# Performance work log

Hardware: AMD Instinct MI355X
Metric: run time of the kernel (lower is better)

The kernel has to match this reference:

```python
import jax, jax.numpy as jnp
import numpy as np

B, T, D, H = 256, 512, 512, 512


def setup_inputs() -> dict:
    key = jax.random.key(0)
    k1, k2, k3, k4 = jax.random.split(key, 4)
    inputs = jax.random.normal(k1, (B, T, D), dtype=jnp.float32)
    lengths = jax.random.randint(k2, (B,), 0, T).astype(jnp.int32)
    # LSTM params. Flax nn.LSTMCell uses per-gate dense layers:
    #  input dense (with bias) and recurrent dense (no bias). Packing the
    #  four gates (i, f, g, o) into one matrix is mathematically identical.
    Wx = jax.random.normal(k3, (D, 4 * H), dtype=jnp.float32) * (1.0 / np.sqrt(D))
    Wh = jax.random.normal(k4, (H, 4 * H), dtype=jnp.float32) * (1.0 / np.sqrt(H))
    b = jnp.zeros((4 * H,), dtype=jnp.float32)
    return {"inputs": inputs, "lengths": lengths, "Wx": Wx, "Wh": Wh, "b": b}


def reference(inputs, lengths, Wx, Wh, b):
    batch = inputs.shape[0]
    hidden = Wh.shape[0]
    x_tbd = jnp.swapaxes(inputs, 0, 1)  # [T, B, D]

    def step(carry, x_t):
        c, h = carry
        # fused gate pre-activations: [B, 4H]
        z = x_t @ Wx + h @ Wh + b
        i, f, g, o = jnp.split(z, 4, axis=-1)
        i = jax.nn.sigmoid(i)
        f = jax.nn.sigmoid(f)
        g = jnp.tanh(g)
        o = jax.nn.sigmoid(o)
        c_new = f * c + i * g
        h_new = o * jnp.tanh(c_new)
        return (c_new, h_new), h_new

    c0 = jnp.zeros((batch, hidden), dtype=inputs.dtype)
    h0 = jnp.zeros((batch, hidden), dtype=inputs.dtype)
    _, hs = jax.lax.scan(step, (c0, h0), x_tbd)  # hs: [T, B, H]

    # select output at last valid timestep per example
    idx = jnp.maximum(0, lengths - 1)  # [B]
    return hs[idx, jnp.arange(batch), :]  # [B, H]
```

## Files before the change

### kernel.cpp

```cpp
#include <hip/hip_runtime.h>

#define Bb 256
#define Tt 512
#define Dd 512
#define Hh 512
#define KTOT 1024
#define FOURH 2048

typedef __attribute__((ext_vector_type(8))) short bf16x8;
typedef __attribute__((ext_vector_type(4))) float f32x4;

__device__ __forceinline__ unsigned short f2bf(float f) {
    union { float f; unsigned u; } x; x.f = f;
    unsigned u = x.u;
    unsigned r = u + 0x7FFFu + ((u >> 16) & 1u);
    return (unsigned short)(r >> 16);
}
__device__ __forceinline__ float bf2f(unsigned short s) {
    union { unsigned u; float f; } x; x.u = ((unsigned)s) << 16;
    return x.f;
}

__device__ __forceinline__ uint4 load16_sc01(const void* p) {
    uint4 v;
    asm volatile("global_load_dwordx4 %0, %1, off sc0 sc1" : "=v"(v) : "v"(p));
    return v;
}

__device__ __forceinline__ void i16_to_bf(int v, unsigned short& bh, unsigned short& bl) {
    int vh = v >> 8;
    int vl = v & 255;
    union { float f; unsigned u; } a, b;
    a.f = (float)vh * 0.0078125f;
    b.f = (float)vl * 3.0517578125e-05f;
    bh = (unsigned short)(a.u >> 16);
    bl = (unsigned short)(b.u >> 16);
}

__global__ void prep_w(const float* __restrict__ Wx, const float* __restrict__ Wh,
                       unsigned short* __restrict__ WT_hi, unsigned short* __restrict__ WT_lo) {
    __shared__ float tile[32][33];
    int n0 = (blockIdx.x & 63) * 32;
    int k0 = (blockIdx.x >> 6) * 32;
    int tx = threadIdx.x & 31;
    int ty = threadIdx.x >> 5;
    for (int q = 0; q < 4; ++q) {
        int k = k0 + ty + q * 8;
        int n = n0 + tx;
        float v = (k < Dd) ? Wx[(size_t)k * FOURH + n] : Wh[(size_t)(k - Dd) * FOURH + n];
        tile[ty + q * 8][tx] = v;
    }
    __syncthreads();
    for (int q = 0; q < 4; ++q) {
        int nl = ty + q * 8;
        int kl = tx;
        float v = tile[kl][nl];
        unsigned short hi = f2bf(v);
        unsigned short lo = f2bf(v - bf2f(hi));
        size_t o = (size_t)(n0 + nl) * KTOT + (size_t)(k0 + kl);
        WT_hi[o] = hi;
        WT_lo[o] = lo;
    }
}

__global__ void init_state3(char* __restrict__ ws, int persist) {
    long i = (long)blockIdx.x * blockDim.x + threadIdx.x;
    if (i < 98304) {
        *(uint4*)(ws + (8u << 20) + i * 16) = (uint4){0, 0, 0, 0};
    }
    if (persist && i < 4096) {
        ((unsigned int*)(ws + (8u << 20) + (1536u << 10)))[i] = 0u;
    }
}

__global__ __launch_bounds__(512) void lstm_persist12(
    const float* __restrict__ X, const int* __restrict__ lengths,
    const unsigned short* __restrict__ WT_hi, const unsigned short* __restrict__ WT_lo,
    const float* __restrict__ bias,
    short* __restrict__ h_i16,
    unsigned int* __restrict__ ctrl,
    float* __restrict__ out)
{
    __shared__ unsigned short HLDS[32768];
    __shared__ unsigned short XLDS[32768];
    __shared__ float zbuf[8][32][17];

    const int bx = blockIdx.x;
    const int group = bx & 7;
    const int slot = bx >> 3;
    const int rt = slot & 7;
    const int cs = slot >> 3;
    const int r0 = rt * 32;
    const int j0h = group * 64 + cs * 16;
    const int tid = threadIdx.x;
    const int w8 = tid >> 6;
    const int lane = tid & 63;
    const int l15 = lane & 15;
    const int q4 = lane >> 4;
    const int klo = q4 * 8;
    const int gate = w8 & 3;
    const int khalf = w8 >> 2;

    const size_t HB = (size_t)Bb * Hh;

    const int colg = gate * 512 + j0h + l15;
    const size_t bbase = (size_t)colg * KTOT + (size_t)khalf * 512;
    const unsigned short* bhp = &WT_hi[bbase];
    const unsigned short* blp = &WT_lo[bbase];

    const int xr = tid >> 4;
    const int xk0 = (tid & 15) * 32;
    const float* xbase = &X[((size_t)(r0 + xr) * Tt) * Dd + xk0];
    const int ksx = tid & 15;
    const int xmi = xr >> 4, xlr = xr & 15;

    const int er = tid >> 4;
    const int ej = tid & 15;
    const int row_g = r0 + er;
    const int col_h = j0h + ej;
    const size_t oidx = (size_t)row_g * Hh + col_h;
    int oT = lengths[row_g] - 1; if (oT < 0) oT = 0;
    const float b0 = bias[col_h], b1 = bias[512 + col_h],
                b2 = bias[1024 + col_h], b3 = bias[1536 + col_h];
    float creg = 0.f;

    const int wgIdx = group * 4 + cs;
    unsigned int* myflag = ctrl + ((size_t)(rt * 32 + wgIdx)) * 16;
    const unsigned int* flagbase = ctrl + (size_t)rt * 32 * 16;
    const unsigned int* pollp = flagbase + (size_t)(lane & 31) * 16;

    {
        const float* xp = xbase;
        float4 xv[8];
#pragma unroll
        for (int i = 0; i < 8; ++i) xv[i] = ((const float4*)xp)[i];
#pragma unroll
        for (int c2 = 0; c2 < 4; ++c2) {
            float vv[8];
            *(float4*)&vv[0] = xv[2 * c2];
            *(float4*)&vv[4] = xv[2 * c2 + 1];
            bf16x8 hv8, lv8;
#pragma unroll
            for (int e = 0; e < 8; ++e) {
                unsigned short hs = f2bf(vv[e]);
                hv8[e] = (short)hs;
                lv8[e] = (short)f2bf(vv[e] - bf2f(hs));
            }
            const int lnw = (c2 * 16 + xlr) ^ (ksx & 7);
            *(bf16x8*)&XLDS[(((0 * 2 + xmi) * 16 + ksx) * 64 + lnw) * 8] = hv8;
            *(bf16x8*)&XLDS[(((1 * 2 + xmi) * 16 + ksx) * 64 + lnw) * 8] = lv8;
        }
    }

    for (int t = 0; t < Tt; ++t) {
        const int p_r = t & 1;
        const short* hp_r = h_i16 + (size_t)p_r * HB;
        short* hp_w = h_i16 + (size_t)(p_r ^ 1) * HB;

        uint4 hb[4];
#pragma unroll
        for (int it = 0; it < 4; ++it) {
            const int c = it * 512 + tid;
            const int row = c >> 6, k8 = c & 63;
            hb[it] = load16_sc01(hp_r + (size_t)(r0 + row) * Hh + k8 * 8);
        }

        asm volatile("s_waitcnt vmcnt(0)" ::: "memory");
        __builtin_amdgcn_sched_barrier(0);

#pragma unroll
        for (int it = 0; it < 4; ++it) {
            const int c = it * 512 + tid;
            const int row = c >> 6, k8 = c & 63;
            const int ksh = k8 >> 2, qq = k8 & 3;
            const int mi = row >> 4, lr = row & 15;
            const uint4 q = hb[it];
            const unsigned qs[4] = {q.x, q.y, q.z, q.w};
            bf16x8 ahv, alv;
#pragma unroll
            for (int e = 0; e < 4; ++e) {
                const unsigned u = qs[e];
                unsigned short bh0, bl0, bh1, bl1;
                i16_to_bf((int)(short)(u & 0xffffu), bh0, bl0);
                i16_to_bf((int)(short)(u >> 16), bh1, bl1);
                ahv[2 * e] = (short)bh0; alv[2 * e] = (short)bl0;
                ahv[2 * e + 1] = (short)bh1; alv[2 * e + 1] = (short)bl1;
            }
            const int lnw = (qq * 16 + lr) ^ (ksh & 7);
            *(bf16x8*)&HLDS[(((0 * 2 + mi) * 16 + ksh) * 64 + lnw) * 8] = ahv;
            *(bf16x8*)&HLDS[(((1 * 2 + mi) * 16 + ksh) * 64 + lnw) * 8] = alv;
        }
        __syncthreads();

        const unsigned short* ALDS = khalf ? HLDS : XLDS;
        f32x4 acc[2][3];
#pragma unroll
        for (int mi = 0; mi < 2; ++mi)
#pragma unroll
            for (int s = 0; s < 3; ++s)
                acc[mi][s] = (f32x4){0.f, 0.f, 0.f, 0.f};

#pragma unroll
        for (int ks = 0; ks < 16; ++ks) {
            const int kk = ks * 32 + klo;
            const bf16x8 bh = *(const bf16x8*)&bhp[kk];
            const bf16x8 bl = *(const bf16x8*)&blp[kk];
            const int lnr = lane ^ (ks & 7);
#pragma unroll
            for (int mi = 0; mi < 2; ++mi) {
                const bf16x8 ah = *(const bf16x8*)&ALDS[(((0 * 2 + mi) * 16 + ks) * 64 + lnr) * 8];
                const bf16x8 al = *(const bf16x8*)&ALDS[(((1 * 2 + mi) * 16 + ks) * 64 + lnr) * 8];
                acc[mi][0] = __builtin_amdgcn_mfma_f32_16x16x32_bf16(ah, bh, acc[mi][0], 0, 0, 0);
                acc[mi][1] = __builtin_amdgcn_mfma_f32_16x16x32_bf16(ah, bl, acc[mi][1], 0, 0, 0);
                acc[mi][2] = __builtin_amdgcn_mfma_f32_16x16x32_bf16(al, bh, acc[mi][2], 0, 0, 0);
            }
        }

#pragma unroll
        for (int mi = 0; mi < 2; ++mi) {
            const f32x4 z = acc[mi][0] + acc[mi][1] + acc[mi][2];
#pragma unroll
            for (int r = 0; r < 4; ++r)
                zbuf[w8][mi * 16 + q4 * 4 + r][l15] = z[r];
        }
        __syncthreads();

        float zi = zbuf[0][er][ej] + zbuf[4][er][ej] + b0;
        float zf = zbuf[1][er][ej] + zbuf[5][er][ej] + b1;
        float zg = zbuf[2][er][ej] + zbuf[6][er][ej] + b2;
        float zo = zbuf[3][er][ej] + zbuf[7][er][ej] + b3;
        float ig = 1.f / (1.f + expf(-zi));
        float fg = 1.f / (1.f + expf(-zf));
        float gg = tanhf(zg);
        float og = 1.f / (1.f + expf(-zo));
        float cn = fg * creg + ig * gg;
        creg = cn;
        float hn = og * tanhf(cn);
        int vi = __float2int_rn(hn * 32768.f);
        vi = vi > 32767 ? 32767 : (vi < -32767 ? -32767 : vi);
        __hip_atomic_store(&hp_w[oidx], (short)vi, __ATOMIC_RELAXED, __HIP_MEMORY_SCOPE_SYSTEM);
        if (t == oT) out[oidx] = hn;

        if (t < Tt - 1) {
            asm volatile("s_waitcnt vmcnt(0)" ::: "memory");
            __syncthreads();
            if (tid == 0)
                __hip_atomic_store(myflag, (unsigned)(t + 1), __ATOMIC_RELAXED,
                                   __HIP_MEMORY_SCOPE_SYSTEM);

            {
                const float* xp = xbase + (size_t)(t + 1) * Dd;
                float4 xv[8];
#pragma unroll
                for (int i = 0; i < 8; ++i) xv[i] = ((const float4*)xp)[i];
#pragma unroll
                for (int c2 = 0; c2 < 4; ++c2) {
                    float vv[8];
                    *(float4*)&vv[0] = xv[2 * c2];
                    *(float4*)&vv[4] = xv[2 * c2 + 1];
                    bf16x8 hv8, lv8;
#pragma unroll
                    for (int e = 0; e < 8; ++e) {
                        unsigned short hs = f2bf(vv[e]);
                        hv8[e] = (short)hs;
                        lv8[e] = (short)f2bf(vv[e] - bf2f(hs));
                    }
                    const int lnw = (c2 * 16 + xlr) ^ (ksx & 7);
                    *(bf16x8*)&XLDS[(((0 * 2 + xmi) * 16 + ksx) * 64 + lnw) * 8] = hv8;
                    *(bf16x8*)&XLDS[(((1 * 2 + xmi) * 16 + ksx) * 64 + lnw) * 8] = lv8;
                }
            }

            if (w8 == 0) {
                while (true) {
                    unsigned v = __hip_atomic_load(pollp, __ATOMIC_RELAXED,
                                                   __HIP_MEMORY_SCOPE_SYSTEM);
                    if (__all(v >= (unsigned)(t + 1))) break;
                    __builtin_amdgcn_s_sleep(2);
                }
            }
            __syncthreads();
        }
    }
}

__global__ __launch_bounds__(512) void lstm_step4(
    const float* __restrict__ X, const int* __restrict__ lengths,
    const unsigned short* __restrict__ WT_hi, const unsigned short* __restrict__ WT_lo,
    const float* __restrict__ bias,
    float* __restrict__ c_st,
    const unsigned short* __restrict__ h_r_hi, const unsigned short* __restrict__ h_r_lo,
    unsigned short* __restrict__ h_w_hi, unsigned short* __restrict__ h_w_lo,
    float* __restrict__ out, int t)
{
    __shared__ float zbuf[8][16][17];

    const int bx = blockIdx.x;
    const int xcd = bx & 7;
    const int rem = bx >> 3;
    const int m0 = (rem & 15) * 16;
    const int col_group = xcd * 4 + (rem >> 4);
    const int hc0 = col_group * 16;
    const int tid = threadIdx.x;
    const int w8 = tid >> 6;
    const int lane = tid & 63;
    const int gate = w8 & 3;
    const int khalf = w8 >> 2;

    f32x4 ahh = (f32x4){0,0,0,0}, ahl = (f32x4){0,0,0,0}, alh = (f32x4){0,0,0,0};

    const int colk = gate * 512 + hc0 + (lane & 15);
    const size_t bbase = (size_t)colk * KTOT;
    const int klo = (lane >> 4) * 8;
    const int row = m0 + (lane & 15);

    if (khalf == 0) {
        const float* xrow = &X[((size_t)row * Tt + t) * Dd];
        const unsigned short* bhp = &WT_hi[bbase];
        const unsigned short* blp = &WT_lo[bbase];
#pragma unroll
        for (int ks = 0; ks < 16; ++ks) {
            const int kk = ks * 32 + klo;
            const float4 v0 = *(const float4*)&xrow[kk];
            const float4 v1 = *(const float4*)&xrow[kk + 4];
            float vv[8] = {v0.x, v0.y, v0.z, v0.w, v1.x, v1.y, v1.z, v1.w};
            bf16x8 ah, al;
#pragma unroll
            for (int e = 0; e < 8; ++e) {
                unsigned short hi = f2bf(vv[e]);
                ah[e] = (short)hi;
                al[e] = (short)f2bf(vv[e] - bf2f(hi));
            }
            const bf16x8 bh = *(const bf16x8*)&bhp[kk];
            const bf16x8 bl = *(const bf16x8*)&blp[kk];
            ahh = __builtin_amdgcn_mfma_f32_16x16x32_bf16(ah, bh, ahh, 0, 0, 0);
            ahl = __builtin_amdgcn_mfma_f32_16x16x32_bf16(ah, bl, ahl, 0, 0, 0);
            alh = __builtin_amdgcn_mfma_f32_16x16x32_bf16(al, bh, alh, 0, 0, 0);
        }
    } else {
        const unsigned short* hrh = &h_r_hi[(size_t)row * Hh];
        const unsigned short* hrl = &h_r_lo[(size_t)row * Hh];
        const unsigned short* bhp = &WT_hi[bbase + 512];
        const unsigned short* blp = &WT_lo[bbase + 512];
#pragma unroll
        for (int ks = 0; ks < 16; ++ks) {
            const int kk = ks * 32 + klo;
            const bf16x8 ah = *(const bf16x8*)&hrh[kk];
            const bf16x8 al = *(const bf16x8*)&hrl[kk];
            const bf16x8 bh = *(const bf16x8*)&bhp[kk];
            const bf16x8 bl = *(const bf16x8*)&blp[kk];
            ahh = __builtin_amdgcn_mfma_f32_16x16x32_bf16(ah, bh, ahh, 0, 0, 0);
            ahl = __builtin_amdgcn_mfma_f32_16x16x32_bf16(ah, bl, ahl, 0, 0, 0);
            alh = __builtin_amdgcn_mfma_f32_16x16x32_bf16(al, bh, alh, 0, 0, 0);
        }
    }

    const f32x4 z = ahh + ahl + alh;
#pragma unroll
    for (int r = 0; r < 4; ++r)
        zbuf[w8][(lane >> 4) * 4 + r][lane & 15] = z[r];
    __syncthreads();

    if (tid < 256) {
        const int r = tid >> 4;
        const int j = tid & 15;
        const int row_g = m0 + r;
        const int col_g = hc0 + j;
        float zi = zbuf[0][r][j] + zbuf[4][r][j] + bias[col_g];
        float zf = zbuf[1][r][j] + zbuf[5][r][j] + bias[512 + col_g];
        float zg = zbuf[2][r][j] + zbuf[6][r][j] + bias[1024 + col_g];
        float zo = zbuf[3][r][j] + zbuf[7][r][j] + bias[1536 + col_g];
        float ig = 1.f / (1.f + expf(-zi));
        float fg = 1.f / (1.f + expf(-zf));
        float gg = tanhf(zg);
        float og = 1.f / (1.f + expf(-zo));
        const size_t idx = (size_t)row_g * Hh + col_g;
        float cn = fg * c_st[idx] + ig * gg;
        float hn = og * tanhf(cn);
        c_st[idx] = cn;
        unsigned short hh = f2bf(hn);
        h_w_hi[idx] = hh;
        h_w_lo[idx] = f2bf(hn - bf2f(hh));
        int len = lengths[row_g];
        int oidx = len - 1; if (oidx < 0) oidx = 0;
        if (t == oidx) out[idx] = hn;
    }
}

extern "C" void kernel_launch(void* const* d_in, const int* in_sizes, int n_in,
                              void* d_out, int out_size, void* d_ws, size_t ws_size,
                              hipStream_t stream) {
    const float* X = (const float*)d_in[0];
    const int* lengths = (const int*)d_in[1];
    const float* Wx = (const float*)d_in[2];
    const float* Wh = (const float*)d_in[3];
    const float* bias = (const float*)d_in[4];
    float* out = (float*)d_out;

    char* ws = (char*)d_ws;
    unsigned short* WT_hi = (unsigned short*)ws;
    unsigned short* WT_lo = (unsigned short*)(ws + (4u << 20));
    short* h_i16 = (short*)(ws + (8u << 20));
    unsigned int* ctrl = (unsigned int*)(ws + (8u << 20) + (1536u << 10));
    float* c_st = (float*)(ws + (8u << 20));
    unsigned short* h_base = (unsigned short*)(ws + (8u << 20) + (512u << 10));
    const size_t HB = (size_t)Bb * Hh;
    unsigned short* h_hi0 = h_base;
    unsigned short* h_lo0 = h_base + HB;
    unsigned short* h_hi1 = h_base + 2 * HB;
    unsigned short* h_lo1 = h_base + 3 * HB;

    const size_t NEED_PERSIST = (8u << 20) + (1536u << 10) + 32768u;
    const int can_persist = (ws_size >= NEED_PERSIST) ? 1 : 0;

    hipLaunchKernelGGL(prep_w, dim3(2048), dim3(256), 0, stream, Wx, Wh, WT_hi, WT_lo);
    hipLaunchKernelGGL(init_state3, dim3(512), dim3(256), 0, stream, ws, can_persist);

    hipError_t err = hipErrorUnknown;
    if (can_persist) {
        void* args[] = { (void*)&X, (void*)&lengths, (void*)&WT_hi, (void*)&WT_lo,
                         (void*)&bias, (void*)&h_i16, (void*)&ctrl, (void*)&out };
        err = hipLaunchCooperativeKernel((const void*)lstm_persist12,
                                         dim3(256), dim3(512), args, 0, stream);
    }
    if (err != hipSuccess) {
        for (int t = 0; t < Tt; ++t) {
            const bool even = (t & 1) == 0;
            hipLaunchKernelGGL(lstm_step4, dim3(512), dim3(512), 0, stream,
                               X, lengths, WT_hi, WT_lo, bias, c_st,
                               even ? h_hi0 : h_hi1, even ? h_lo0 : h_lo1,
                               even ? h_hi1 : h_hi0, even ? h_lo1 : h_lo0,
                               out, t);
        }
    }
}
```

Measured before the change: 6.112 ms.

## Replace flag barrier with tagged hidden-state values for per-element readiness polling

Removes the per-workgroup flag counters and the group-wide poll barrier. Each hidden value now carries a 1-bit parity tag in its LSB, and readers spin on the h data itself, reloading only stale chunks until all tags match the expected phase. The next step's h loads are issued right after the store, before the X conversion, so their latency overlaps. The cost is one bit of hidden-state quantization precision (15-bit instead of 16-bit) and a reliance on tag parity, which depends on double buffering to avoid ABA confusion.

```diff
diff --git a/kernel.cpp b/kernel.cpp
--- a/kernel.cpp
+++ b/kernel.cpp
@@ -27,12 +27,13 @@
     return v;
 }
 
-__device__ __forceinline__ void i16_to_bf(int v, unsigned short& bh, unsigned short& bl) {
-    int vh = v >> 8;
-    int vl = v & 255;
+__device__ __forceinline__ void s16tag_to_bf(int s, unsigned short& bh, unsigned short& bl) {
+    int vq = s >> 1;
+    int vh = vq >> 7;
+    int vl = vq & 127;
     union { float f; unsigned u; } a, b;
     a.f = (float)vh * 0.0078125f;
-    b.f = (float)vl * 3.0517578125e-05f;
+    b.f = (float)vl * 6.103515625e-05f;
     bh = (unsigned short)(a.u >> 16);
     bl = (unsigned short)(b.u >> 16);
 }
@@ -63,22 +64,21 @@
     }
 }
 
-__global__ void init_state3(char* __restrict__ ws, int persist) {
+__global__ void init_state5(char* __restrict__ ws, int persist) {
     long i = (long)blockIdx.x * blockDim.x + threadIdx.x;
     if (i < 98304) {
-        *(uint4*)(ws + (8u << 20) + i * 16) = (uint4){0, 0, 0, 0};
-    }
-    if (persist && i < 4096) {
-        ((unsigned int*)(ws + (8u << 20) + (1536u << 10)))[i] = 0u;
-    }
-}
-
-__global__ __launch_bounds__(512) void lstm_persist12(
+        uint4 v = (uint4){0, 0, 0, 0};
+        if (persist && i >= 16384 && i < 32768)
+            v = (uint4){0x00010001u, 0x00010001u, 0x00010001u, 0x00010001u};
+        *(uint4*)(ws + (8u << 20) + i * 16) = v;
+    }
+}
+
+__global__ __launch_bounds__(512) void lstm_persist14(
     const float* __restrict__ X, const int* __restrict__ lengths,
     const unsigned short* __restrict__ WT_hi, const unsigned short* __restrict__ WT_lo,
     const float* __restrict__ bias,
     short* __restrict__ h_i16,
-    unsigned int* __restrict__ ctrl,
     float* __restrict__ out)
 {
     __shared__ unsigned short HLDS[32768];
@@ -124,11 +124,6 @@
                 b2 = bias[1024 + col_h], b3 = bias[1536 + col_h];
     float creg = 0.f;
 
-    const int wgIdx = group * 4 + cs;
-    unsigned int* myflag = ctrl + ((size_t)(rt * 32 + wgIdx)) * 16;
-    const unsigned int* flagbase = ctrl + (size_t)rt * 32 * 16;
-    const unsigned int* pollp = flagbase + (size_t)(lane & 31) * 16;
-
     {
         const float* xp = xbase;
         float4 xv[8];
@@ -152,21 +147,45 @@
         }
     }
 
+    uint4 hb[4];
+    {
+        const short* hp0 = h_i16;
+#pragma unroll
+        for (int it = 0; it < 4; ++it) {
+            const int c = it * 512 + tid;
+            const int row = c >> 6, k8 = c & 63;
+            hb[it] = load16_sc01(hp0 + (size_t)(r0 + row) * Hh + k8 * 8);
+        }
+    }
+
     for (int t = 0; t < Tt; ++t) {
         const int p_r = t & 1;
         const short* hp_r = h_i16 + (size_t)p_r * HB;
         short* hp_w = h_i16 + (size_t)(p_r ^ 1) * HB;
-
-        uint4 hb[4];
-#pragma unroll
-        for (int it = 0; it < 4; ++it) {
-            const int c = it * 512 + tid;
-            const int row = c >> 6, k8 = c & 63;
-            hb[it] = load16_sc01(hp_r + (size_t)(r0 + row) * Hh + k8 * 8);
-        }
-
-        asm volatile("s_waitcnt vmcnt(0)" ::: "memory");
-        __builtin_amdgcn_sched_barrier(0);
+        const unsigned expTag = (unsigned)((t >> 1) & 1);
+        const unsigned tagpat = expTag ? 0x00010001u : 0u;
+
+        while (true) {
+            asm volatile("s_waitcnt vmcnt(0)" ::: "memory");
+            __builtin_amdgcn_sched_barrier(0);
+            unsigned stale = 0;
+#pragma unroll
+            for (int it = 0; it < 4; ++it) {
+                unsigned d = ((hb[it].x ^ tagpat) | (hb[it].y ^ tagpat) |
+                              (hb[it].z ^ tagpat) | (hb[it].w ^ tagpat)) & 0x00010001u;
+                if (d) stale |= (1u << it);
+            }
+            if (!__any(stale != 0)) break;
+#pragma unroll
+            for (int it = 0; it < 4; ++it) {
+                if (stale & (1u << it)) {
+                    const int c = it * 512 + tid;
+                    const int row = c >> 6, k8 = c & 63;
+                    hb[it] = load16_sc01(hp_r + (size_t)(r0 + row) * Hh + k8 * 8);
+                }
+            }
+            __builtin_amdgcn_s_sleep(4);
+        }
 
 #pragma unroll
         for (int it = 0; it < 4; ++it) {
@@ -181,8 +200,8 @@
             for (int e = 0; e < 4; ++e) {
                 const unsigned u = qs[e];
                 unsigned short bh0, bl0, bh1, bl1;
-                i16_to_bf((int)(short)(u & 0xffffu), bh0, bl0);
-                i16_to_bf((int)(short)(u >> 16), bh1, bl1);
+                s16tag_to_bf((int)(short)(u & 0xffffu), bh0, bl0);
+                s16tag_to_bf((int)(short)(u >> 16), bh1, bl1);
                 ahv[2 * e] = (short)bh0; alv[2 * e] = (short)bl0;
                 ahv[2 * e + 1] = (short)bh1; alv[2 * e + 1] = (short)bl1;
             }
@@ -236,50 +255,42 @@
         float cn = fg * creg + ig * gg;
         creg = cn;
         float hn = og * tanhf(cn);
-        int vi = __float2int_rn(hn * 32768.f);
-        vi = vi > 32767 ? 32767 : (vi < -32767 ? -32767 : vi);
-        __hip_atomic_store(&hp_w[oidx], (short)vi, __ATOMIC_RELAXED, __HIP_MEMORY_SCOPE_SYSTEM);
+        int vi = __float2int_rn(hn * 16384.f);
+        vi = vi > 16383 ? 16383 : (vi < -16383 ? -16383 : vi);
+        const unsigned tagNext = (unsigned)(((t + 1) >> 1) & 1);
+        short sv = (short)((vi << 1) | (int)tagNext);
+        __hip_atomic_store(&hp_w[oidx], sv, __ATOMIC_RELAXED, __HIP_MEMORY_SCOPE_SYSTEM);
         if (t == oT) out[oidx] = hn;
 
         if (t < Tt - 1) {
-            asm volatile("s_waitcnt vmcnt(0)" ::: "memory");
-            __syncthreads();
-            if (tid == 0)
-                __hip_atomic_store(myflag, (unsigned)(t + 1), __ATOMIC_RELAXED,
-                                   __HIP_MEMORY_SCOPE_SYSTEM);
-
-            {
-                const float* xp = xbase + (size_t)(t + 1) * Dd;
-                float4 xv[8];
-#pragma unroll
-                for (int i = 0; i < 8; ++i) xv[i] = ((const float4*)xp)[i];
-#pragma unroll
-                for (int c2 = 0; c2 < 4; ++c2) {
-                    float vv[8];
-                    *(float4*)&vv[0] = xv[2 * c2];
-                    *(float4*)&vv[4] = xv[2 * c2 + 1];
-                    bf16x8 hv8, lv8;
-#pragma unroll
-                    for (int e = 0; e < 8; ++e) {
-                        unsigned short hs = f2bf(vv[e]);
-                        hv8[e] = (short)hs;
-                        lv8[e] = (short)f2bf(vv[e] - bf2f(hs));
-                    }
-                    const int lnw = (c2 * 16 + xlr) ^ (ksx & 7);
-                    *(bf16x8*)&XLDS[(((0 * 2 + xmi) * 16 + ksx) * 64 + lnw) * 8] = hv8;
-                    *(bf16x8*)&XLDS[(((1 * 2 + xmi) * 16 + ksx) * 64 + lnw) * 8] = lv8;
+            const short* hp_n = h_i16 + (size_t)((t + 1) & 1) * HB;
+#pragma unroll
+            for (int it = 0; it < 4; ++it) {
+                const int c = it * 512 + tid;
+                const int row = c >> 6, k8 = c & 63;
+                hb[it] = load16_sc01(hp_n + (size_t)(r0 + row) * Hh + k8 * 8);
+            }
+
+            const float* xp = xbase + (size_t)(t + 1) * Dd;
+            float4 xv[8];
+#pragma unroll
+            for (int i = 0; i < 8; ++i) xv[i] = ((const float4*)xp)[i];
+#pragma unroll
+            for (int c2 = 0; c2 < 4; ++c2) {
+                float vv[8];
+                *(float4*)&vv[0] = xv[2 * c2];
+                *(float4*)&vv[4] = xv[2 * c2 + 1];
+                bf16x8 hv8, lv8;
+#pragma unroll
+                for (int e = 0; e < 8; ++e) {
+                    unsigned short hs = f2bf(vv[e]);
+                    hv8[e] = (short)hs;
+                    lv8[e] = (short)f2bf(vv[e] - bf2f(hs));
                 }
-            }
-
-            if (w8 == 0) {
-                while (true) {
-                    unsigned v = __hip_atomic_load(pollp, __ATOMIC_RELAXED,
-                                                   __HIP_MEMORY_SCOPE_SYSTEM);
-                    if (__all(v >= (unsigned)(t + 1))) break;
-                    __builtin_amdgcn_s_sleep(2);
-                }
-            }
-            __syncthreads();
+                const int lnw = (c2 * 16 + xlr) ^ (ksx & 7);
+                *(bf16x8*)&XLDS[(((0 * 2 + xmi) * 16 + ksx) * 64 + lnw) * 8] = hv8;
+                *(bf16x8*)&XLDS[(((1 * 2 + xmi) * 16 + ksx) * 64 + lnw) * 8] = lv8;
+            }
         }
     }
 }
@@ -401,7 +412,6 @@
     unsigned short* WT_hi = (unsigned short*)ws;
     unsigned short* WT_lo = (unsigned short*)(ws + (4u << 20));
     short* h_i16 = (short*)(ws + (8u << 20));
-    unsigned int* ctrl = (unsigned int*)(ws + (8u << 20) + (1536u << 10));
     float* c_st = (float*)(ws + (8u << 20));
     unsigned short* h_base = (unsigned short*)(ws + (8u << 20) + (512u << 10));
     const size_t HB = (size_t)Bb * Hh;
@@ -414,13 +424,13 @@
     const int can_persist = (ws_size >= NEED_PERSIST) ? 1 : 0;
 
     hipLaunchKernelGGL(prep_w, dim3(2048), dim3(256), 0, stream, Wx, Wh, WT_hi, WT_lo);
-    hipLaunchKernelGGL(init_state3, dim3(512), dim3(256), 0, stream, ws, can_persist);
+    hipLaunchKernelGGL(init_state5, dim3(512), dim3(256), 0, stream, ws, can_persist);
 
     hipError_t err = hipErrorUnknown;
     if (can_persist) {
         void* args[] = { (void*)&X, (void*)&lengths, (void*)&WT_hi, (void*)&WT_lo,
-                         (void*)&bias, (void*)&h_i16, (void*)&ctrl, (void*)&out };
-        err = hipLaunchCooperativeKernel((const void*)lstm_persist12,
+                         (void*)&bias, (void*)&h_i16, (void*)&out };
+        err = hipLaunchCooperativeKernel((const void*)lstm_persist14,
                                          dim3(256), dim3(512), args, 0, stream);
     }
     if (err != hipSuccess) {
```

New measurement: 6.417 ms. +5.0%, slower.

## Split recurrent h load into two halves to overlap conversion with MFMA

Applied to the files above, without the earlier changes.

Each step's h-state load is split into two K-halves. The first half is waited on, converted and staged into LDS. The h-path warps then compute on it while the second half's loads are still in flight, and the x-path warps run their full 16-step product. This is meant to hide the global-memory latency of the second half of h behind MFMA work. It adds an extra __syncthreads per timestep and uneven work between the x and h warp groups.

```diff
diff --git a/kernel.cpp b/kernel.cpp
--- a/kernel.cpp
+++ b/kernel.cpp
@@ -73,7 +73,7 @@
     }
 }
 
-__global__ __launch_bounds__(512) void lstm_persist12(
+__global__ __launch_bounds__(512) void lstm_persist15(
     const float* __restrict__ X, const int* __restrict__ lengths,
     const unsigned short* __restrict__ WT_hi, const unsigned short* __restrict__ WT_lo,
     const float* __restrict__ bias,
@@ -114,6 +114,11 @@
     const int ksx = tid & 15;
     const int xmi = xr >> 4, xlr = xr & 15;
 
+    const int hrow0 = (2 * tid) >> 5;
+    const int hrow1 = (2 * tid + 1) >> 5;
+    const int hk0 = (2 * tid) & 31;
+    const int hk1 = (2 * tid + 1) & 31;
+
     const int er = tid >> 4;
     const int ej = tid & 15;
     const int row_g = r0 + er;
@@ -158,23 +163,20 @@
         short* hp_w = h_i16 + (size_t)(p_r ^ 1) * HB;
 
         uint4 hb[4];
-#pragma unroll
-        for (int it = 0; it < 4; ++it) {
-            const int c = it * 512 + tid;
-            const int row = c >> 6, k8 = c & 63;
-            hb[it] = load16_sc01(hp_r + (size_t)(r0 + row) * Hh + k8 * 8);
-        }
-
-        asm volatile("s_waitcnt vmcnt(0)" ::: "memory");
+        hb[0] = load16_sc01(hp_r + (size_t)(r0 + hrow0) * Hh + hk0 * 8);
+        hb[1] = load16_sc01(hp_r + (size_t)(r0 + hrow1) * Hh + hk1 * 8);
+        hb[2] = load16_sc01(hp_r + (size_t)(r0 + hrow0) * Hh + (32 + hk0) * 8);
+        hb[3] = load16_sc01(hp_r + (size_t)(r0 + hrow1) * Hh + (32 + hk1) * 8);
+
+        asm volatile("s_waitcnt vmcnt(2)" ::: "memory");
         __builtin_amdgcn_sched_barrier(0);
-
-#pragma unroll
-        for (int it = 0; it < 4; ++it) {
-            const int c = it * 512 + tid;
-            const int row = c >> 6, k8 = c & 63;
+#pragma unroll
+        for (int b = 0; b < 2; ++b) {
+            const int row = b ? hrow1 : hrow0;
+            const int k8 = b ? hk1 : hk0;
             const int ksh = k8 >> 2, qq = k8 & 3;
             const int mi = row >> 4, lr = row & 15;
-            const uint4 q = hb[it];
+            const uint4 q = hb[b];
             const unsigned qs[4] = {q.x, q.y, q.z, q.w};
             bf16x8 ahv, alv;
 #pragma unroll
@@ -192,7 +194,6 @@
         }
         __syncthreads();
 
-        const unsigned short* ALDS = khalf ? HLDS : XLDS;
         f32x4 acc[2][3];
 #pragma unroll
         for (int mi = 0; mi < 2; ++mi)
@@ -200,28 +201,96 @@
             for (int s = 0; s < 3; ++s)
                 acc[mi][s] = (f32x4){0.f, 0.f, 0.f, 0.f};
 
-#pragma unroll
-        for (int ks = 0; ks < 16; ++ks) {
-            const int kk = ks * 32 + klo;
-            const bf16x8 bh = *(const bf16x8*)&bhp[kk];
-            const bf16x8 bl = *(const bf16x8*)&blp[kk];
-            const int lnr = lane ^ (ks & 7);
+        if (khalf == 0) {
+#pragma unroll
+            for (int ks = 0; ks < 16; ++ks) {
+                const int kk = ks * 32 + klo;
+                const bf16x8 bh = *(const bf16x8*)&bhp[kk];
+                const bf16x8 bl = *(const bf16x8*)&blp[kk];
+                const int lnr = lane ^ (ks & 7);
+#pragma unroll
+                for (int mi = 0; mi < 2; ++mi) {
+                    const bf16x8 ah = *(const bf16x8*)&XLDS[(((0 * 2 + mi) * 16 + ks) * 64 + lnr) * 8];
+                    const bf16x8 al = *(const bf16x8*)&XLDS[(((1 * 2 + mi) * 16 + ks) * 64 + lnr) * 8];
+                    acc[mi][0] = __builtin_amdgcn_mfma_f32_16x16x32_bf16(ah, bh, acc[mi][0], 0, 0, 0);
+                    acc[mi][1] = __builtin_amdgcn_mfma_f32_16x16x32_bf16(ah, bl, acc[mi][1], 0, 0, 0);
+                    acc[mi][2] = __builtin_amdgcn_mfma_f32_16x16x32_bf16(al, bh, acc[mi][2], 0, 0, 0);
+                }
+            }
 #pragma unroll
             for (int mi = 0; mi < 2; ++mi) {
-                const bf16x8 ah = *(const bf16x8*)&ALDS[(((0 * 2 + mi) * 16 + ks) * 64 + lnr) * 8];
-                const bf16x8 al = *(const bf16x8*)&ALDS[(((1 * 2 + mi) * 16 + ks) * 64 + lnr) * 8];
-                acc[mi][0] = __builtin_amdgcn_mfma_f32_16x16x32_bf16(ah, bh, acc[mi][0], 0, 0, 0);
-                acc[mi][1] = __builtin_amdgcn_mfma_f32_16x16x32_bf16(ah, bl, acc[mi][1], 0, 0, 0);
-                acc[mi][2] = __builtin_amdgcn_mfma_f32_16x16x32_bf16(al, bh, acc[mi][2], 0, 0, 0);
-            }
-        }
-
-#pragma unroll
-        for (int mi = 0; mi < 2; ++mi) {
-            const f32x4 z = acc[mi][0] + acc[mi][1] + acc[mi][2];
-#pragma unroll
-            for (int r = 0; r < 4; ++r)
-                zbuf[w8][mi * 16 + q4 * 4 + r][l15] = z[r];
+                const f32x4 z = acc[mi][0] + acc[mi][1] + acc[mi][2];
+#pragma unroll
+                for (int r = 0; r < 4; ++r)
+                    zbuf[w8][mi * 16 + q4 * 4 + r][l15] = z[r];
+            }
+        } else {
+#pragma unroll
+            for (int ks = 0; ks < 8; ++ks) {
+                const int kk = ks * 32 + klo;
+                const bf16x8 bh = *(const bf16x8*)&bhp[kk];
+                const bf16x8 bl = *(const bf16x8*)&blp[kk];
+                const int lnr = lane ^ (ks & 7);
+#pragma unroll
+                for (int mi = 0; mi < 2; ++mi) {
+                    const bf16x8 ah = *(const bf16x8*)&HLDS[(((0 * 2 + mi) * 16 + ks) * 64 + lnr) * 8];
+                    const bf16x8 al = *(const bf16x8*)&HLDS[(((1 * 2 + mi) * 16 + ks) * 64 + lnr) * 8];
+                    acc[mi][0] = __builtin_amdgcn_mfma_f32_16x16x32_bf16(ah, bh, acc[mi][0], 0, 0, 0);
+                    acc[mi][1] = __builtin_amdgcn_mfma_f32_16x16x32_bf16(ah, bl, acc[mi][1], 0, 0, 0);
+                    acc[mi][2] = __builtin_amdgcn_mfma_f32_16x16x32_bf16(al, bh, acc[mi][2], 0, 0, 0);
+                }
+            }
+        }
+
+        asm volatile("s_waitcnt vmcnt(0)" ::: "memory");
+        __builtin_amdgcn_sched_barrier(0);
+#pragma unroll
+        for (int b = 0; b < 2; ++b) {
+            const int row = b ? hrow1 : hrow0;
+            const int k8 = 32 + (b ? hk1 : hk0);
+            const int ksh = k8 >> 2, qq = k8 & 3;
+            const int mi = row >> 4, lr = row & 15;
+            const uint4 q = hb[2 + b];
+            const unsigned qs[4] = {q.x, q.y, q.z, q.w};
+            bf16x8 ahv, alv;
+#pragma unroll
+            for (int e = 0; e < 4; ++e) {
+                const unsigned u = qs[e];
+                unsigned short bh0, bl0, bh1, bl1;
+                i16_to_bf((int)(short)(u & 0xffffu), bh0, bl0);
+                i16_to_bf((int)(short)(u >> 16), bh1, bl1);
+                ahv[2 * e] = (short)bh0; alv[2 * e] = (short)bl0;
+                ahv[2 * e + 1] = (short)bh1; alv[2 * e + 1] = (short)bl1;
+            }
+            const int lnw = (qq * 16 + lr) ^ (ksh & 7);
+            *(bf16x8*)&HLDS[(((0 * 2 + mi) * 16 + ksh) * 64 + lnw) * 8] = ahv;
+            *(bf16x8*)&HLDS[(((1 * 2 + mi) * 16 + ksh) * 64 + lnw) * 8] = alv;
+        }
+        __syncthreads();
+
+        if (khalf == 1) {
+#pragma unroll
+            for (int ks = 8; ks < 16; ++ks) {
+                const int kk = ks * 32 + klo;
+                const bf16x8 bh = *(const bf16x8*)&bhp[kk];
+                const bf16x8 bl = *(const bf16x8*)&blp[kk];
+                const int lnr = lane ^ (ks & 7);
+#pragma unroll
+                for (int mi = 0; mi < 2; ++mi) {
+                    const bf16x8 ah = *(const bf16x8*)&HLDS[(((0 * 2 + mi) * 16 + ks) * 64 + lnr) * 8];
+                    const bf16x8 al = *(const bf16x8*)&HLDS[(((1 * 2 + mi) * 16 + ks) * 64 + lnr) * 8];
+                    acc[mi][0] = __builtin_amdgcn_mfma_f32_16x16x32_bf16(ah, bh, acc[mi][0], 0, 0, 0);
+                    acc[mi][1] = __builtin_amdgcn_mfma_f32_16x16x32_bf16(ah, bl, acc[mi][1], 0, 0, 0);
+                    acc[mi][2] = __builtin_amdgcn_mfma_f32_16x16x32_bf16(al, bh, acc[mi][2], 0, 0, 0);
+                }
+            }
+#pragma unroll
+            for (int mi = 0; mi < 2; ++mi) {
+                const f32x4 z = acc[mi][0] + acc[mi][1] + acc[mi][2];
+#pragma unroll
+                for (int r = 0; r < 4; ++r)
+                    zbuf[w8][mi * 16 + q4 * 4 + r][l15] = z[r];
+            }
         }
         __syncthreads();
 
@@ -420,7 +489,7 @@
     if (can_persist) {
         void* args[] = { (void*)&X, (void*)&lengths, (void*)&WT_hi, (void*)&WT_lo,
                          (void*)&bias, (void*)&h_i16, (void*)&ctrl, (void*)&out };
-        err = hipLaunchCooperativeKernel((const void*)lstm_persist12,
+        err = hipLaunchCooperativeKernel((const void*)lstm_persist15,
                                          dim3(256), dim3(512), args, 0, stream);
     }
     if (err != hipSuccess) {
```

After: 6.099 ms. About the same (-0.2%).

## Move input-projection GEMM off the recurrent critical path into the barrier wait

Applied to the files above, without the earlier changes.

The per-step work is restructured so the x·Wx partial products for step t+1 are computed by waves 1-7 while wave 0 spins on the grid barrier, and stored in a separate zxbuf. After the barrier only the h·Wh GEMM remains on the critical path, split across all 8 waves over K. The next h tile load is also issued right after the barrier, overlapping with wave 0's late x GEMM. This adds extra LDS syncs, a second z buffer, and a serial x GEMM on wave 0 after the barrier, which could delay the next step.

```diff
diff --git a/kernel.cpp b/kernel.cpp
--- a/kernel.cpp
+++ b/kernel.cpp
@@ -73,7 +73,7 @@
     }
 }
 
-__global__ __launch_bounds__(512) void lstm_persist12(
+__global__ __launch_bounds__(512) void lstm_persist16(
     const float* __restrict__ X, const int* __restrict__ lengths,
     const unsigned short* __restrict__ WT_hi, const unsigned short* __restrict__ WT_lo,
     const float* __restrict__ bias,
@@ -81,9 +81,9 @@
     unsigned int* __restrict__ ctrl,
     float* __restrict__ out)
 {
-    __shared__ unsigned short HLDS[32768];
-    __shared__ unsigned short XLDS[32768];
+    __shared__ unsigned short ALDS[32768];
     __shared__ float zbuf[8][32][17];
+    __shared__ float zxbuf[8][32][17];
 
     const int bx = blockIdx.x;
     const int group = bx & 7;
@@ -99,14 +99,15 @@
     const int q4 = lane >> 4;
     const int klo = q4 * 8;
     const int gate = w8 & 3;
-    const int khalf = w8 >> 2;
+    const int ksub = w8 >> 2;
 
     const size_t HB = (size_t)Bb * Hh;
 
     const int colg = gate * 512 + j0h + l15;
-    const size_t bbase = (size_t)colg * KTOT + (size_t)khalf * 512;
-    const unsigned short* bhp = &WT_hi[bbase];
-    const unsigned short* blp = &WT_lo[bbase];
+    const unsigned short* bhp_h = &WT_hi[(size_t)colg * KTOT + 512];
+    const unsigned short* blp_h = &WT_lo[(size_t)colg * KTOT + 512];
+    const unsigned short* bhp_x = &WT_hi[(size_t)colg * KTOT];
+    const unsigned short* blp_x = &WT_lo[(size_t)colg * KTOT];
 
     const int xr = tid >> 4;
     const int xk0 = (tid & 15) * 32;
@@ -147,24 +148,53 @@
                 lv8[e] = (short)f2bf(vv[e] - bf2f(hs));
             }
             const int lnw = (c2 * 16 + xlr) ^ (ksx & 7);
-            *(bf16x8*)&XLDS[(((0 * 2 + xmi) * 16 + ksx) * 64 + lnw) * 8] = hv8;
-            *(bf16x8*)&XLDS[(((1 * 2 + xmi) * 16 + ksx) * 64 + lnw) * 8] = lv8;
-        }
+            *(bf16x8*)&ALDS[(((0 * 2 + xmi) * 16 + ksx) * 64 + lnw) * 8] = hv8;
+            *(bf16x8*)&ALDS[(((1 * 2 + xmi) * 16 + ksx) * 64 + lnw) * 8] = lv8;
+        }
+    }
+    __syncthreads();
+    {
+        f32x4 acc[2][3];
+#pragma unroll
+        for (int mi = 0; mi < 2; ++mi)
+#pragma unroll
+            for (int s = 0; s < 3; ++s) acc[mi][s] = (f32x4){0, 0, 0, 0};
+#pragma unroll
+        for (int j = 0; j < 8; ++j) {
+            const int ks = ksub * 8 + j;
+            const int kk = ks * 32 + klo;
+            const bf16x8 bh = *(const bf16x8*)&bhp_x[kk];
+            const bf16x8 bl = *(const bf16x8*)&blp_x[kk];
+            const int lnr = lane ^ (ks & 7);
+#pragma unroll
+            for (int mi = 0; mi < 2; ++mi) {
+                const bf16x8 ah = *(const bf16x8*)&ALDS[(((0 * 2 + mi) * 16 + ks) * 64 + lnr) * 8];
+                const bf16x8 al = *(const bf16x8*)&ALDS[(((1 * 2 + mi) * 16 + ks) * 64 + lnr) * 8];
+                acc[mi][0] = __builtin_amdgcn_mfma_f32_16x16x32_bf16(ah, bh, acc[mi][0], 0, 0, 0);
+                acc[mi][1] = __builtin_amdgcn_mfma_f32_16x16x32_bf16(ah, bl, acc[mi][1], 0, 0, 0);
+                acc[mi][2] = __builtin_amdgcn_mfma_f32_16x16x32_bf16(al, bh, acc[mi][2], 0, 0, 0);
+            }
+        }
+#pragma unroll
+        for (int mi = 0; mi < 2; ++mi) {
+            const f32x4 z = acc[mi][0] + acc[mi][1] + acc[mi][2];
+#pragma unroll
+            for (int r = 0; r < 4; ++r)
+                zxbuf[w8][mi * 16 + q4 * 4 + r][l15] = z[r];
+        }
+    }
+    uint4 hb[4];
+#pragma unroll
+    for (int it = 0; it < 4; ++it) {
+        const int c = it * 512 + tid;
+        const int row = c >> 6, k8 = c & 63;
+        hb[it] = load16_sc01(h_i16 + (size_t)(r0 + row) * Hh + k8 * 8);
     }
 
     for (int t = 0; t < Tt; ++t) {
-        const int p_r = t & 1;
-        const short* hp_r = h_i16 + (size_t)p_r * HB;
-        short* hp_w = h_i16 + (size_t)(p_r ^ 1) * HB;
-
-        uint4 hb[4];
-#pragma unroll
-        for (int it = 0; it < 4; ++it) {
-            const int c = it * 512 + tid;
-            const int row = c >> 6, k8 = c & 63;
-            hb[it] = load16_sc01(hp_r + (size_t)(r0 + row) * Hh + k8 * 8);
-        }
-
+        short* hp_w = h_i16 + (size_t)((t ^ 1) & 1) * HB;
+
+        __syncthreads();
         asm volatile("s_waitcnt vmcnt(0)" ::: "memory");
         __builtin_amdgcn_sched_barrier(0);
 
@@ -187,48 +217,47 @@
                 ahv[2 * e + 1] = (short)bh1; alv[2 * e + 1] = (short)bl1;
             }
             const int lnw = (qq * 16 + lr) ^ (ksh & 7);
-            *(bf16x8*)&HLDS[(((0 * 2 + mi) * 16 + ksh) * 64 + lnw) * 8] = ahv;
-            *(bf16x8*)&HLDS[(((1 * 2 + mi) * 16 + ksh) * 64 + lnw) * 8] = alv;
+            *(bf16x8*)&ALDS[(((0 * 2 + mi) * 16 + ksh) * 64 + lnw) * 8] = ahv;
+            *(bf16x8*)&ALDS[(((1 * 2 + mi) * 16 + ksh) * 64 + lnw) * 8] = alv;
         }
         __syncthreads();
 
-        const unsigned short* ALDS = khalf ? HLDS : XLDS;
-        f32x4 acc[2][3];
-#pragma unroll
-        for (int mi = 0; mi < 2; ++mi)
-#pragma unroll
-            for (int s = 0; s < 3; ++s)
-                acc[mi][s] = (f32x4){0.f, 0.f, 0.f, 0.f};
-
-#pragma unroll
-        for (int ks = 0; ks < 16; ++ks) {
-            const int kk = ks * 32 + klo;
-            const bf16x8 bh = *(const bf16x8*)&bhp[kk];
-            const bf16x8 bl = *(const bf16x8*)&blp[kk];
-            const int lnr = lane ^ (ks & 7);
+        {
+            f32x4 acc[2][3];
+#pragma unroll
+            for (int mi = 0; mi < 2; ++mi)
+#pragma unroll
+                for (int s = 0; s < 3; ++s) acc[mi][s] = (f32x4){0, 0, 0, 0};
+#pragma unroll
+            for (int j = 0; j < 8; ++j) {
+                const int ks = ksub * 8 + j;
+                const int kk = ks * 32 + klo;
+                const bf16x8 bh = *(const bf16x8*)&bhp_h[kk];
+                const bf16x8 bl = *(const bf16x8*)&blp_h[kk];
+                const int lnr = lane ^ (ks & 7);
+#pragma unroll
+                for (int mi = 0; mi < 2; ++mi) {
+                    const bf16x8 ah = *(const bf16x8*)&ALDS[(((0 * 2 + mi) * 16 + ks) * 64 + lnr) * 8];
+                    const bf16x8 al = *(const bf16x8*)&ALDS[(((1 * 2 + mi) * 16 + ks) * 64 + lnr) * 8];
+                    acc[mi][0] = __builtin_amdgcn_mfma_f32_16x16x32_bf16(ah, bh, acc[mi][0], 0, 0, 0);
+                    acc[mi][1] = __builtin_amdgcn_mfma_f32_16x16x32_bf16(ah, bl, acc[mi][1], 0, 0, 0);
+                    acc[mi][2] = __builtin_amdgcn_mfma_f32_16x16x32_bf16(al, bh, acc[mi][2], 0, 0, 0);
+                }
+            }
 #pragma unroll
             for (int mi = 0; mi < 2; ++mi) {
-                const bf16x8 ah = *(const bf16x8*)&ALDS[(((0 * 2 + mi) * 16 + ks) * 64 + lnr) * 8];
-                const bf16x8 al = *(const bf16x8*)&ALDS[(((1 * 2 + mi) * 16 + ks) * 64 + lnr) * 8];
-                acc[mi][0] = __builtin_amdgcn_mfma_f32_16x16x32_bf16(ah, bh, acc[mi][0], 0, 0, 0);
-                acc[mi][1] = __builtin_amdgcn_mfma_f32_16x16x32_bf16(ah, bl, acc[mi][1], 0, 0, 0);
-                acc[mi][2] = __builtin_amdgcn_mfma_f32_16x16x32_bf16(al, bh, acc[mi][2], 0, 0, 0);
-            }
-        }
-
-#pragma unroll
-        for (int mi = 0; mi < 2; ++mi) {
-            const f32x4 z = acc[mi][0] + acc[mi][1] + acc[mi][2];
-#pragma unroll
-            for (int r = 0; r < 4; ++r)
-                zbuf[w8][mi * 16 + q4 * 4 + r][l15] = z[r];
+                const f32x4 z = acc[mi][0] + acc[mi][1] + acc[mi][2];
+#pragma unroll
+                for (int r = 0; r < 4; ++r)
+                    zbuf[w8][mi * 16 + q4 * 4 + r][l15] = z[r];
+            }
         }
         __syncthreads();
 
-        float zi = zbuf[0][er][ej] + zbuf[4][er][ej] + b0;
-        float zf = zbuf[1][er][ej] + zbuf[5][er][ej] + b1;
-        float zg = zbuf[2][er][ej] + zbuf[6][er][ej] + b2;
-        float zo = zbuf[3][er][ej] + zbuf[7][er][ej] + b3;
+        float zi = zbuf[0][er][ej] + zbuf[4][er][ej] + zxbuf[0][er][ej] + zxbuf[4][er][ej] + b0;
+        float zf = zbuf[1][er][ej] + zbuf[5][er][ej] + zxbuf[1][er][ej] + zxbuf[5][er][ej] + b1;
+        float zg = zbuf[2][er][ej] + zbuf[6][er][ej] + zxbuf[2][er][ej] + zxbuf[6][er][ej] + b2;
+        float zo = zbuf[3][er][ej] + zbuf[7][er][ej] + zxbuf[3][er][ej] + zxbuf[7][er][ej] + b3;
         float ig = 1.f / (1.f + expf(-zi));
         float fg = 1.f / (1.f + expf(-zf));
         float gg = tanhf(zg);
@@ -266,10 +295,17 @@
                         lv8[e] = (short)f2bf(vv[e] - bf2f(hs));
                     }
                     const int lnw = (c2 * 16 + xlr) ^ (ksx & 7);
-                    *(bf16x8*)&XLDS[(((0 * 2 + xmi) * 16 + ksx) * 64 + lnw) * 8] = hv8;
-                    *(bf16x8*)&XLDS[(((1 * 2 + xmi) * 16 + ksx) * 64 + lnw) * 8] = lv8;
-                }
-            }
+                    *(bf16x8*)&ALDS[(((0 * 2 + xmi) * 16 + ksx) * 64 + lnw) * 8] = hv8;
+                    *(bf16x8*)&ALDS[(((1 * 2 + xmi) * 16 + ksx) * 64 + lnw) * 8] = lv8;
+                }
+            }
+            __syncthreads();
+
+            f32x4 acc[2][3];
+#pragma unroll
+            for (int mi = 0; mi < 2; ++mi)
+#pragma unroll
+                for (int s = 0; s < 3; ++s) acc[mi][s] = (f32x4){0, 0, 0, 0};
 
             if (w8 == 0) {
                 while (true) {
@@ -278,8 +314,66 @@
                     if (__all(v >= (unsigned)(t + 1))) break;
                     __builtin_amdgcn_s_sleep(2);
                 }
+            } else {
+#pragma unroll
+                for (int j = 0; j < 8; ++j) {
+                    const int ks = ksub * 8 + j;
+                    const int kk = ks * 32 + klo;
+                    const bf16x8 bh = *(const bf16x8*)&bhp_x[kk];
+                    const bf16x8 bl = *(const bf16x8*)&blp_x[kk];
+                    const int lnr = lane ^ (ks & 7);
+#pragma unroll
+                    for (int mi = 0; mi < 2; ++mi) {
+                        const bf16x8 ah = *(const bf16x8*)&ALDS[(((0 * 2 + mi) * 16 + ks) * 64 + lnr) * 8];
+                        const bf16x8 al = *(const bf16x8*)&ALDS[(((1 * 2 + mi) * 16 + ks) * 64 + lnr) * 8];
+                        acc[mi][0] = __builtin_amdgcn_mfma_f32_16x16x32_bf16(ah, bh, acc[mi][0], 0, 0, 0);
+                        acc[mi][1] = __builtin_amdgcn_mfma_f32_16x16x32_bf16(ah, bl, acc[mi][1], 0, 0, 0);
+                        acc[mi][2] = __builtin_amdgcn_mfma_f32_16x16x32_bf16(al, bh, acc[mi][2], 0, 0, 0);
+                    }
+                }
+#pragma unroll
+                for (int mi = 0; mi < 2; ++mi) {
+                    const f32x4 z = acc[mi][0] + acc[mi][1] + acc[mi][2];
+#pragma unroll
+                    for (int r = 0; r < 4; ++r)
+                        zxbuf[w8][mi * 16 + q4 * 4 + r][l15] = z[r];
+                }
             }
             __syncthreads();
+
+            const short* hp_n = h_i16 + (size_t)((t + 1) & 1) * HB;
+#pragma unroll
+            for (int it = 0; it < 4; ++it) {
+                const int c = it * 512 + tid;
+                const int row = c >> 6, k8 = c & 63;
+                hb[it] = load16_sc01(hp_n + (size_t)(r0 + row) * Hh + k8 * 8);
+            }
+
+            if (w8 == 0) {
+#pragma unroll
+                for (int j = 0; j < 8; ++j) {
+                    const int ks = ksub * 8 + j;
+                    const int kk = ks * 32 + klo;
+                    const bf16x8 bh = *(const bf16x8*)&bhp_x[kk];
+                    const bf16x8 bl = *(const bf16x8*)&blp_x[kk];
+                    const int lnr = lane ^ (ks & 7);
+#pragma unroll
+                    for (int mi = 0; mi < 2; ++mi) {
+                        const bf16x8 ah = *(const bf16x8*)&ALDS[(((0 * 2 + mi) * 16 + ks) * 64 + lnr) * 8];
+                        const bf16x8 al = *(const bf16x8*)&ALDS[(((1 * 2 + mi) * 16 + ks) * 64 + lnr) * 8];
+                        acc[mi][0] = __builtin_amdgcn_mfma_f32_16x16x32_bf16(ah, bh, acc[mi][0], 0, 0, 0);
+                        acc[mi][1] = __builtin_amdgcn_mfma_f32_16x16x32_bf16(ah, bl, acc[mi][1], 0, 0, 0);
+                        acc[mi][2] = __builtin_amdgcn_mfma_f32_16x16x32_bf16(al, bh, acc[mi][2], 0, 0, 0);
+                    }
+                }
+#pragma unroll
+                for (int mi = 0; mi < 2; ++mi) {
+                    const f32x4 z = acc[mi][0] + acc[mi][1] + acc[mi][2];
+#pragma unroll
+                    for (int r = 0; r < 4; ++r)
+                        zxbuf[w8][mi * 16 + q4 * 4 + r][l15] = z[r];
+                }
+            }
         }
     }
 }
@@ -420,7 +514,7 @@
     if (can_persist) {
         void* args[] = { (void*)&X, (void*)&lengths, (void*)&WT_hi, (void*)&WT_lo,
                          (void*)&bias, (void*)&h_i16, (void*)&ctrl, (void*)&out };
-        err = hipLaunchCooperativeKernel((const void*)lstm_persist12,
+        err = hipLaunchCooperativeKernel((const void*)lstm_persist16,
                                          dim3(256), dim3(512), args, 0, stream);
     }
     if (err != hipSuccess) {
```

Result: slower. 6.562 ms (+7.4%).
